# Kernel tuning notes

Measured on AMD Instinct MI355X. Metric: run time of the kernel, lower is better.

Reference implementation:

```python
import jax, jax.numpy as jnp
import numpy as np

N_NODES = 100000
N_EDGES = 500000
D = 128
D_OUT = 128


def setup_inputs() -> dict:
    key = jax.random.key(0)
    k1, k2, k3, k4, k5 = jax.random.split(key, 5)
    x = jax.random.normal(k1, (N_NODES, D), dtype=jnp.float32)
    pos_edge_index = jax.random.randint(k2, (2, N_EDGES), 0, N_NODES, dtype=jnp.int64)
    neg_edge_index = jax.random.randint(k3, (2, N_EDGES), 0, N_NODES, dtype=jnp.int64)
    W = jax.random.normal(k4, (3 * D, D_OUT), dtype=jnp.float32) * (1.0 / np.sqrt(3 * D))
    b = jax.random.normal(k5, (D_OUT,), dtype=jnp.float32) * 0.01
    return {"x": x, "pos_edge_index": pos_edge_index, "neg_edge_index": neg_edge_index, "W": W, "b": b}


def _agg(x, edge_index):
    # PyG add-aggregation: message x_j gathered from source (row 0),
    # scatter-added to destination (row 1).
    src, dst = edge_index[0], edge_index[1]
    return jax.ops.segment_sum(x[src], dst, num_segments=x.shape[0])


def reference(x, pos_edge_index, neg_edge_index, W, b):
    x_pos = _agg(x, pos_edge_index)  # [N, D]
    x_neg = _agg(x, neg_edge_index)  # [N, D]
    out_cat = jnp.concatenate((x, x_pos, x_neg), axis=1)  # [N, 3D]
    return out_cat @ W + b  # [N, D_OUT]
```

## Files before the change

kernel.cpp:

```cpp
#include <hip/hip_runtime.h>

#define NNODES 100000
#define NEDGES 500000
#define DD 128
#define NBUK 1563
#define BCAP 896
#define BINB 123
#define ZBYTE ((unsigned int)NNODES << 8)

typedef __attribute__((ext_vector_type(8))) short short8v;
typedef __attribute__((ext_vector_type(4))) float f32x4;

__device__ __forceinline__ unsigned short f2bf(float f) {
    unsigned int u = __float_as_uint(f);
    return (unsigned short)((u + 0x7FFFu + ((u >> 16) & 1u)) >> 16);
}
__device__ __forceinline__ unsigned int f2bf2(float a, float b) {
    return (unsigned int)f2bf(a) | ((unsigned int)f2bf(b) << 16);
}
__device__ __forceinline__ float bflo(unsigned int v) {
    return __uint_as_float(v << 16);
}
__device__ __forceinline__ float bfhi(unsigned int v) {
    return __uint_as_float(v & 0xFFFF0000u);
}

__global__ __launch_bounds__(256) void init_kernel(
        int* __restrict__ gcur, const unsigned int* __restrict__ e,
        int* __restrict__ flag) {
    if (blockIdx.x < 7) {
        const int i = blockIdx.x * 256 + threadIdx.x;
        if (i < NBUK) gcur[i] = 0;
        return;
    }
    __shared__ unsigned int s_acc;
    if (threadIdx.x == 0) s_acc = 0u;
    __syncthreads();
    unsigned int v = 0u;
    for (int i = threadIdx.x; i < 4096; i += 256)
        v |= e[2 * i + 1];
    for (int off = 32; off > 0; off >>= 1)
        v |= __shfl_down(v, off, 64);
    if ((threadIdx.x & 63) == 0) atomicOr(&s_acc, v);
    __syncthreads();
    if (threadIdx.x == 0) *flag = (s_acc == 0u) ? 1 : 0;
}

__global__ __launch_bounds__(256) void prep_kernel(
        const float4* __restrict__ x4, uint2* __restrict__ xb2,
        const float* __restrict__ W, unsigned short* __restrict__ wb,
        const void* __restrict__ pe, const void* __restrict__ ne,
        const int* __restrict__ flag,
        int* __restrict__ gcur, unsigned int* __restrict__ regions) {
    const int b = blockIdx.x;
    if (b < BINB) {
        __shared__ int hist[NBUK];
        __shared__ int gbase[NBUK];
        const int tid = threadIdx.x;
        for (int i = tid; i < NBUK; i += 256) hist[i] = 0;
        __syncthreads();
        const int e0 = b * 8192;
        const int fl = *flag;
        for (int k0 = 0; k0 < 32; k0 += 8) {
            int dv[8];
            bool ok[8];
#pragma unroll
            for (int j = 0; j < 8; ++j) {
                const int i = e0 + (k0 + j) * 256 + tid;
                ok[j] = i < 2 * NEDGES;
                const int ic = ok[j] ? i : 0;
                const int list = ic >= NEDGES;
                const int e = ic - list * NEDGES;
                const void* ed = list ? ne : pe;
                dv[j] = fl ? (int)((const long long*)ed)[NEDGES + e]
                           : ((const int*)ed)[NEDGES + e];
            }
#pragma unroll
            for (int j = 0; j < 8; ++j)
                if (ok[j]) atomicAdd(&hist[dv[j] >> 6], 1);
        }
        __syncthreads();
        for (int i = tid; i < NBUK; i += 256) {
            const int h = hist[i];
            gbase[i] = h ? atomicAdd(&gcur[i], h) : 0;
            hist[i] = 0;
        }
        __syncthreads();
        for (int k0 = 0; k0 < 32; k0 += 8) {
            unsigned int ent[8];
            int bk[8];
            bool ok[8];
#pragma unroll
            for (int j = 0; j < 8; ++j) {
                const int i = e0 + (k0 + j) * 256 + tid;
                ok[j] = i < 2 * NEDGES;
                const int ic = ok[j] ? i : 0;
                const int list = ic >= NEDGES;
                const int e = ic - list * NEDGES;
                int s, d;
                if (fl) {
                    const long long* p = (const long long*)(list ? ne : pe);
                    s = (int)p[e]; d = (int)p[NEDGES + e];
                } else {
                    const int* p = (const int*)(list ? ne : pe);
                    s = p[e]; d = p[NEDGES + e];
                }
                bk[j] = d >> 6;
                ent[j] = ((unsigned int)s << 7) |
                         ((unsigned int)(d & 63) << 1) | (unsigned int)list;
            }
            int pos[8];
#pragma unroll
            for (int j = 0; j < 8; ++j)
                if (ok[j]) pos[j] = gbase[bk[j]] + atomicAdd(&hist[bk[j]], 1);
#pragma unroll
            for (int j = 0; j < 8; ++j)
                if (ok[j] && pos[j] < BCAP)
                    regions[(size_t)bk[j] * BCAP + pos[j]] = ent[j];
        }
    } else if (b < BINB + 24) {
        const int t = (b - BINB) * 256 + threadIdx.x;
        const int l = t & 63;
        const int nf = (t >> 6) & 7;
        const int s = t >> 9;
        const int n = nf * 16 + (l & 15);
        const int k0 = s * 32 + (l >> 4) * 8;
        unsigned short* o = wb + (size_t)t * 8;
#pragma unroll
        for (int j = 0; j < 8; ++j)
            o[j] = f2bf(W[(size_t)(k0 + j) * DD + n]);
    } else if (b == BINB + 24) {
        if (threadIdx.x < 64)
            ((unsigned int*)xb2)[(size_t)NNODES * 64 + threadIdx.x] = 0u;
    } else {
        const int n = NNODES * DD / 4;
        for (int i = (b - BINB - 25) * 256 + threadIdx.x; i < n; i += 512 * 256) {
            const float4 v = x4[i];
            uint2 o;
            o.x = f2bf2(v.x, v.y);
            o.y = f2bf2(v.z, v.w);
            xb2[i] = o;
        }
    }
}

__global__ __launch_bounds__(512) void aggemm_kernel(
        const char* __restrict__ xbb,
        const int* __restrict__ gcur, const unsigned int* __restrict__ regions,
        const unsigned short* __restrict__ wb,
        const float* __restrict__ bias,
        float* __restrict__ out) {
    __shared__ unsigned short tile[64 * 264];
    __shared__ unsigned int sorted[BCAP];
    __shared__ int cnt[128];
    __shared__ int tmp[128];
    __shared__ int sstart[129];
    __shared__ int scur[128];

    const int b = blockIdx.x;
    const int node0 = b * 64;
    const int tid = threadIdx.x;
    const int wid = tid >> 6;
    const int lane = tid & 63;

    int n = gcur[b];
    n = n < BCAP ? n : BCAP;
    const unsigned int* __restrict__ reg = regions + (size_t)b * BCAP;

    if (tid < 128) cnt[tid] = 0;
    __syncthreads();
    for (int i = tid; i < n; i += 512)
        atomicAdd(&cnt[reg[i] & 127u], 1);
    __syncthreads();
    if (tid < 128) tmp[tid] = cnt[tid];
    __syncthreads();
#pragma unroll
    for (int off = 1; off < 128; off <<= 1) {
        int v = 0;
        if (tid < 128 && tid >= off) v = tmp[tid - off];
        __syncthreads();
        if (tid < 128) tmp[tid] += v;
        __syncthreads();
    }
    if (tid < 128) {
        const int st = tmp[tid] - cnt[tid];
        sstart[tid] = st;
        scur[tid] = st;
    }
    if (tid == 127) sstart[128] = tmp[127];
    __syncthreads();
    for (int i = tid; i < n; i += 512) {
        const unsigned int ent = reg[i];
        const int pos = atomicAdd(&scur[ent & 127u], 1);
        sorted[pos] = (ent >> 7) << 8;
    }
    __syncthreads();

    const unsigned int lane4 = lane * 4;
    unsigned int* tileW = (unsigned int*)tile;
#pragma unroll 1
    for (int k = 0; k < 16; ++k) {
        const int seg = wid * 16 + k;
        const int s0 = sstart[seg], s1 = sstart[seg + 1];
        float ax = 0.f, ay = 0.f;
        for (int base = s0; base < s1; base += 8) {
            unsigned int off[8];
#pragma unroll
            for (int j = 0; j < 8; ++j) {
                const int ii = base + j;
                off[j] = (ii < s1) ? sorted[ii] : ZBYTE;
            }
            unsigned int v[8];
#pragma unroll
            for (int j = 0; j < 8; ++j)
                v[j] = *(const unsigned int*)(xbb + (size_t)(off[j] + lane4));
#pragma unroll
            for (int j = 0; j < 8; ++j) {
                ax += bflo(v[j]);
                ay += bfhi(v[j]);
            }
        }
        tileW[(seg >> 1) * 132 + (seg & 1) * 64 + lane] = f2bf2(ax, ay);
    }
    __syncthreads();

    const int lm = lane & 15;
    const int lk = lane >> 4;
    const int rg = wid & 3;
    const int ch = wid >> 2;
    const int rl0 = rg * 16;
    f32x4 acc[4];
#pragma unroll
    for (int nf = 0; nf < 4; ++nf) acc[nf] = (f32x4)(0.f);

    int rowg = node0 + rl0 + lm;
    if (rowg > NNODES) rowg = NNODES;
    const unsigned short* __restrict__ xb = (const unsigned short*)xbb;

    for (int c = 0; c < 3; ++c) {
#pragma unroll
        for (int s = 0; s < 4; ++s) {
            short8v a;
            if (c == 0)
                a = *(const short8v*)(xb + (size_t)rowg * 128 + s * 32 + lk * 8);
            else
                a = *(const short8v*)(tile + (rl0 + lm) * 264 +
                                      (c - 1) * 128 + s * 32 + lk * 8);
            const short8v* __restrict__ bp =
                (const short8v*)wb + ((size_t)((c * 4 + s) * 8 + ch * 4)) * 64 + lane;
#pragma unroll
            for (int nf = 0; nf < 4; ++nf)
                acc[nf] = __builtin_amdgcn_mfma_f32_16x16x32_bf16(
                    a, bp[nf * 64], acc[nf], 0, 0, 0);
        }
    }

    const int rbase = node0 + rl0 + lk * 4;
#pragma unroll
    for (int nf = 0; nf < 4; ++nf) {
        const int col = (ch * 4 + nf) * 16 + lm;
        const float bv = bias[col];
#pragma unroll
        for (int r = 0; r < 4; ++r) {
            const int row = rbase + r;
            if (row < NNODES)
                out[(size_t)row * 128 + col] = acc[nf][r] + bv;
        }
    }
}

extern "C" void kernel_launch(void* const* d_in, const int* in_sizes, int n_in,
                              void* d_out, int out_size, void* d_ws, size_t ws_size,
                              hipStream_t stream) {
    const float* x     = (const float*)d_in[0];
    const void*  pos_e = d_in[1];
    const void*  neg_e = d_in[2];
    const float* W     = (const float*)d_in[3];
    const float* bias  = (const float*)d_in[4];
    float*       out   = (float*)d_out;

    const size_t XB = ((size_t)NNODES + 1) * DD * 2;
    const size_t WB = 12 * 8 * 64 * 8 * 2;
    const size_t GB = 8192;
    const size_t RB = (size_t)NBUK * BCAP * 4;

    char* ws = (char*)d_ws;
    int* flag = (int*)ws;
    size_t off = 256;
    unsigned int*   xb      = (unsigned int*)(ws + off);   off += XB;
    unsigned short* wb      = (unsigned short*)(ws + off); off += WB;
    int*            gcur    = (int*)(ws + off);            off += GB;
    unsigned int*   regions = (unsigned int*)(ws + off);   off += RB;
    (void)ws_size;

    init_kernel<<<8, 256, 0, stream>>>(gcur, (const unsigned int*)pos_e, flag);

    prep_kernel<<<BINB + 25 + 512, 256, 0, stream>>>(
        (const float4*)x, (uint2*)xb, W, wb, pos_e, neg_e, flag, gcur, regions);

    aggemm_kernel<<<NBUK, 512, 0, stream>>>(
        (const char*)xb, gcur, regions, wb, bias, out);
}
```

Before: 102.5 us.

## Gather each warp's 16 segments in one flattened pass with segment tags

```diff
diff --git a/kernel.cpp b/kernel.cpp
--- a/kernel.cpp
+++ b/kernel.cpp
@@ -192,35 +192,7 @@
     for (int i = tid; i < n; i += 512) {
         const unsigned int ent = reg[i];
         const int pos = atomicAdd(&scur[ent & 127u], 1);
-        sorted[pos] = (ent >> 7) << 8;
-    }
-    __syncthreads();
-
-    const unsigned int lane4 = lane * 4;
-    unsigned int* tileW = (unsigned int*)tile;
-#pragma unroll 1
-    for (int k = 0; k < 16; ++k) {
-        const int seg = wid * 16 + k;
-        const int s0 = sstart[seg], s1 = sstart[seg + 1];
-        float ax = 0.f, ay = 0.f;
-        for (int base = s0; base < s1; base += 8) {
-            unsigned int off[8];
-#pragma unroll
-            for (int j = 0; j < 8; ++j) {
-                const int ii = base + j;
-                off[j] = (ii < s1) ? sorted[ii] : ZBYTE;
-            }
-            unsigned int v[8];
-#pragma unroll
-            for (int j = 0; j < 8; ++j)
-                v[j] = *(const unsigned int*)(xbb + (size_t)(off[j] + lane4));
-#pragma unroll
-            for (int j = 0; j < 8; ++j) {
-                ax += bflo(v[j]);
-                ay += bfhi(v[j]);
-            }
-        }
-        tileW[(seg >> 1) * 132 + (seg & 1) * 64 + lane] = f2bf2(ax, ay);
+        sorted[pos] = ((ent >> 7) << 8) | (ent & 127u);
     }
     __syncthreads();
 
@@ -229,20 +201,72 @@
     const int rg = wid & 3;
     const int ch = wid >> 2;
     const int rl0 = rg * 16;
-    f32x4 acc[4];
-#pragma unroll
-    for (int nf = 0; nf < 4; ++nf) acc[nf] = (f32x4)(0.f);
-
     int rowg = node0 + rl0 + lm;
     if (rowg > NNODES) rowg = NNODES;
     const unsigned short* __restrict__ xb = (const unsigned short*)xbb;
+    short8v a0pre[4];
+#pragma unroll
+    for (int s = 0; s < 4; ++s)
+        a0pre[s] = *(const short8v*)(xb + (size_t)rowg * 128 + s * 32 + lk * 8);
+
+    unsigned int* tileW = (unsigned int*)tile;
+#pragma unroll
+    for (int r = 0; r < 8; ++r) {
+        tileW[(wid * 8 + r) * 132 + lane] = 0u;
+        tileW[(wid * 8 + r) * 132 + 64 + lane] = 0u;
+    }
+    const int lo = sstart[wid * 16];
+    const int hi = sstart[wid * 16 + 16];
+    const unsigned int lane4 = lane * 4;
+    unsigned int cur = 255u;
+    float ax = 0.f, ay = 0.f;
+    for (int base = lo; base < hi; base += 8) {
+        unsigned int ent[8];
+#pragma unroll
+        for (int j = 0; j < 8; ++j) {
+            const int ii = base + j;
+            ent[j] = (ii < hi) ? sorted[ii] : (ZBYTE | 255u);
+        }
+        unsigned int v[8];
+#pragma unroll
+        for (int j = 0; j < 8; ++j)
+            v[j] = *(const unsigned int*)(
+                xbb + (size_t)((ent[j] & 0xFFFFFF00u) + lane4));
+#pragma unroll
+        for (int j = 0; j < 8; ++j) {
+            const unsigned int s = ent[j] & 255u;
+            if (s != cur) {
+                if (cur != 255u) {
+                    unsigned int* w =
+                        &tileW[(cur >> 1) * 132 + (cur & 1) * 64 + lane];
+                    const unsigned int o = *w;
+                    *w = f2bf2(bflo(o) + ax, bfhi(o) + ay);
+                }
+                cur = s;
+                ax = 0.f;
+                ay = 0.f;
+            }
+            ax += bflo(v[j]);
+            ay += bfhi(v[j]);
+        }
+    }
+    if (cur != 255u) {
+        unsigned int* w = &tileW[(cur >> 1) * 132 + (cur & 1) * 64 + lane];
+        const unsigned int o = *w;
+        *w = f2bf2(bflo(o) + ax, bfhi(o) + ay);
+    }
+    __syncthreads();
+
+    f32x4 acc[4];
+#pragma unroll
+    for (int nf = 0; nf < 4; ++nf) acc[nf] = (f32x4)(0.f);
 
     for (int c = 0; c < 3; ++c) {
 #pragma unroll
         for (int s = 0; s < 4; ++s) {
             short8v a;
             if (c == 0)
-                a = *(const short8v*)(xb + (size_t)rowg * 128 + s * 32 + lk * 8);
+                a = a0pre[s];
             else
                 a = *(const short8v*)(tile + (rl0 + lm) * 264 +
                                       (c - 1) * 128 + s * 32 + lk * 8);
```

After: 100.1 us. -2.3%, faster.
